# Kernel tuning notes

Measured on AMD Instinct MI355X. Metric: run time of the kernel, lower is better.

Reference implementation:

```python
import jax, jax.numpy as jnp
import numpy as np

B, C, H, W = 8, 128, 64, 64


def setup_inputs() -> dict:
    key = jax.random.key(0)
    ks = jax.random.split(key, 7)
    query_img = jax.random.normal(ks[0], (B, C, H, W), dtype=jnp.float32)
    key_img = jax.random.normal(ks[1], (B, C, H, W), dtype=jnp.float32)
    value_img = jax.random.normal(ks[2], (B, C, H, W), dtype=jnp.float32)
    # 1x1 conv weights == dense [out, in] matrices (kaiming-ish scale)
    scale = 1.0 / np.sqrt(C)
    Wq = jax.random.normal(ks[3], (C, C), dtype=jnp.float32) * scale
    bq = jax.random.normal(ks[4], (C,), dtype=jnp.float32) * scale
    Wk = jax.random.normal(ks[5], (C, C), dtype=jnp.float32) * scale
    bk = jax.random.normal(ks[6], (C,), dtype=jnp.float32) * scale
    return {"query_img": query_img, "key_img": key_img, "value_img": value_img,
            "Wq": Wq, "bq": bq, "Wk": Wk, "bk": bk}


def reference(query_img, key_img, value_img, Wq, bq, Wk, bk):
    b, c, h, w = query_img.shape
    hw = h * w
    # 1x1 convs as GEMMs -> token-major layout (b, hw, c_out)
    q = jnp.einsum('bchw,oc->bhwo', query_img, Wq).reshape(b, hw, -1) + bq
    k = jnp.einsum('bchw,oc->bohw', key_img, Wk).reshape(b, -1, hw) + bk[None, :, None]
    # scores scaled by sqrt(HW) (faithful: key.size(-1) == h*w in source)
    scores = jnp.einsum('bqc,bck->bqk', q, k) / jnp.sqrt(jnp.float32(hw))
    attn = jax.nn.softmax(scores, axis=-1)  # (b, hw, hw)
    v = value_img.reshape(b, c, hw).transpose(0, 2, 1)  # (b, hw, c)
    out = jnp.einsum('bqk,bkc->bqc', attn, v)  # (b, hw, c)
    out = out.transpose(0, 2, 1).reshape(b, -1, h, w)
    out = out + q.transpose(0, 2, 1).reshape(b, -1, h, w)  # residual from query proj
    return out
```

## Files before the change

kernel.cpp:

```cpp
#include <hip/hip_runtime.h>

#define BB 8
#define CC 128
#define SS 4096
#define KT 64
#define SCALE 0.015625f

typedef __attribute__((ext_vector_type(8))) short sh8;
typedef __attribute__((ext_vector_type(4))) float f32x4;

__device__ __forceinline__ float b2f(unsigned short u) {
    union { unsigned int i; float f; } x; x.i = ((unsigned int)u) << 16; return x.f;
}
__device__ __forceinline__ unsigned short f2b(float f) {
    union { float f; unsigned int i; } x; x.f = f;
    unsigned int r = x.i + 0x7fff + ((x.i >> 16) & 1);
    return (unsigned short)(r >> 16);
}
__device__ __forceinline__ unsigned short rhu(float f) {
    union { float f; unsigned int i; } x; x.f = f;
    return (unsigned short)((x.i + 0x8000) >> 16);
}

__device__ __forceinline__ void dma16(const void* g, void* l) {
    __builtin_amdgcn_global_load_lds((const __attribute__((address_space(1))) void*)g,
                                     (__attribute__((address_space(3))) void*)l,
                                     16, 0, 0);
}

__global__ __launch_bounds__(256) void cvt_kernel(
    const float* __restrict__ vimg,
    const float* __restrict__ Wq, const float* __restrict__ Wk,
    const float* __restrict__ bq, const float* __restrict__ bk,
    unsigned short* __restrict__ Vbuf,
    unsigned short* __restrict__ Wqb, unsigned short* __restrict__ Wkb,
    unsigned short* __restrict__ bqb, unsigned short* __restrict__ bkb)
{
    const int bx = blockIdx.x, tid = threadIdx.x;
    if (bx < 512) {
        const size_t base = (size_t)bx * 8192 + tid * 4;
        #pragma unroll
        for (int it = 0; it < 8; ++it) {
            const size_t i = base + (size_t)it * 1024;
            float4 v = *(const float4*)(vimg + i);
            ushort4 o;
            o.x = f2b(v.x); o.y = f2b(v.y); o.z = f2b(v.z); o.w = f2b(v.w);
            *(ushort4*)(Vbuf + i) = o;
        }
    } else {
        const int w = bx - 512;
        for (int e = w * 256 + tid; e < 33024; e += 2048) {
            float v; unsigned short* dst;
            if (e < 16384)      { v = Wq[e];         dst = Wqb + e; }
            else if (e < 32768) { v = Wk[e - 16384]; dst = Wkb + (e - 16384); }
            else if (e < 32896) { v = bq[e - 32768]; dst = bqb + (e - 32768); }
            else                { v = bk[e - 32896]; dst = bkb + (e - 32896); }
            *dst = f2b(v);
        }
    }
}

__global__ __launch_bounds__(256) void proj_kernel(
    const float* __restrict__ qimg, const float* __restrict__ kimg,
    const unsigned short* __restrict__ Wqb, const unsigned short* __restrict__ Wkb,
    const unsigned short* __restrict__ bqb, const unsigned short* __restrict__ bkb,
    unsigned short* __restrict__ Qbuf, unsigned short* __restrict__ Kbuf)
{
    __shared__ float ilds[128 * 69];

    const int z = blockIdx.z;
    const float* img = (z == 0) ? qimg : kimg;
    const unsigned short* Wb = (z == 0) ? Wqb : Wkb;
    const unsigned short* bias = (z == 0) ? bqb : bkb;
    unsigned short* outTok = (z == 0) ? Qbuf : Kbuf;

    const int tid  = threadIdx.x;
    const int wave = tid >> 6;
    const int lane = tid & 63;
    const int l15  = lane & 15;
    const int quad = lane >> 4;
    const int b     = blockIdx.y;
    const int stile = blockIdx.x;

    const float* gbase = img + (size_t)b * CC * SS + stile * 64;
    #pragma unroll
    for (int i = 0; i < 8; ++i) {
        const int l = tid + 256 * i;
        const int row = l >> 4, col = (l & 15) * 4;
        float4 v = *(const float4*)(gbase + (size_t)row * SS + col);
        float* d = ilds + row * 69 + col;
        d[0] = v.x; d[1] = v.y; d[2] = v.z; d[3] = v.w;
    }
    __syncthreads();

    const int tcol = wave * 16 + l15;
    sh8 a[4];
    #pragma unroll
    for (int kk = 0; kk < 4; ++kk)
        #pragma unroll
        for (int j = 0; j < 8; ++j)
            a[kk][j] = (short)rhu(ilds[(32 * kk + quad * 8 + j) * 69 + tcol]);

    f32x4 acc[8];
    #pragma unroll
    for (int nt = 0; nt < 8; ++nt) acc[nt] = (f32x4){0.f, 0.f, 0.f, 0.f};

    #pragma unroll
    for (int nt = 0; nt < 8; ++nt) {
        const unsigned short* wp = Wb + (size_t)(16 * nt + l15) * CC + quad * 8;
        #pragma unroll
        for (int kk = 0; kk < 4; ++kk) {
            sh8 bf = *(const sh8*)(wp + 32 * kk);
            acc[nt] = __builtin_amdgcn_mfma_f32_16x16x32_bf16(a[kk], bf, acc[nt], 0, 0, 0);
        }
    }

    #pragma unroll
    for (int nt = 0; nt < 8; ++nt) {
        const int o = 16 * nt + l15;
        const float bv = b2f(bias[o]);
        #pragma unroll
        for (int r = 0; r < 4; ++r) {
            const int s = stile * 64 + wave * 16 + quad * 4 + r;
            outTok[((size_t)b * SS + s) * CC + o] = f2b(acc[nt][r] + bv);
        }
    }
}

__global__ __launch_bounds__(256, 4) void attn_kernel(
    const unsigned short* __restrict__ Qbuf,
    const unsigned short* __restrict__ Kbuf,
    const unsigned short* __restrict__ Vbuf,
    float* __restrict__ out)
{
    __shared__ __align__(16) unsigned char smem[40960];
    unsigned char* kb = smem;
    unsigned char* vb = smem + 16384;

    const int tid  = threadIdx.x;
    const int wave = tid >> 6;
    const int lane = tid & 63;
    const int l15  = lane & 15;
    const int quad = lane >> 4;
    const int b     = blockIdx.y;
    const int qtile = blockIdx.x;
    const int qbase = qtile * 64 + wave * 16;

    unsigned char* pw = smem + 32768 + wave * 2048;

    const unsigned short* kbp = Kbuf + (size_t)b * SS * CC;
    const unsigned short* vbp = Vbuf + (size_t)b * CC * SS;

    sh8 aq[4];
    {
        const unsigned short* qp = Qbuf + ((size_t)b * SS + qbase + l15) * CC + quad * 8;
        #pragma unroll
        for (int kk = 0; kk < 4; ++kk) aq[kk] = *(const sh8*)(qp + 32 * kk);
    }

    int kGO[4], vGO[4];
    #pragma unroll
    for (int j = 0; j < 4; ++j) {
        const int krow = wave * 16 + j * 4 + (lane >> 4);
        kGO[j] = krow * 256 + (((lane & 15) ^ (krow & 7)) << 4);
        const int vrow = (wave * 4 + j) * 8 + (lane >> 3);
        vGO[j] = vrow * 8192 + (((lane & 7) ^ ((lane >> 3) & 7)) << 4);
    }

    f32x4 oacc[8];
    #pragma unroll
    for (int ct = 0; ct < 8; ++ct) oacc[ct] = (f32x4){0.f, 0.f, 0.f, 0.f};
    float lsum[4] = {0.f, 0.f, 0.f, 0.f};

    #pragma unroll
    for (int j = 0; j < 4; ++j) {
        dma16((const char*)kbp + kGO[j], kb + (wave * 4 + j) * 1024);
        dma16((const char*)vbp + vGO[j], vb + (wave * 4 + j) * 1024);
    }

    for (int it = 0; it < SS / KT; ++it) {
        __syncthreads();

        f32x4 sacc[4];
        #pragma unroll
        for (int n = 0; n < 4; ++n) {
            sacc[n] = (f32x4){0.f, 0.f, 0.f, 0.f};
            #pragma unroll
            for (int kk = 0; kk < 4; ++kk) {
                sh8 kf = *(const sh8*)(kb + (16 * n + l15) * 256
                                          + (((4 * kk + quad) ^ (l15 & 7)) << 4));
                sacc[n] = __builtin_amdgcn_mfma_f32_16x16x32_bf16(aq[kk], kf, sacc[n], 0, 0, 0);
            }
        }

        #pragma unroll
        for (int n = 0; n < 4; ++n)
            #pragma unroll
            for (int r = 0; r < 4; ++r) {
                float p = __expf(sacc[n][r] * SCALE);
                lsum[r] += p;
                const int row = quad * 4 + r, col = 16 * n + l15;
                *(unsigned short*)(pw + row * 128
                                   + (((col >> 3) ^ (row & 7)) << 4)
                                   + (col & 7) * 2) = rhu(p);
            }

        sh8 ap0 = *(const sh8*)(pw + l15 * 128 + ((quad ^ (l15 & 7)) << 4));
        #pragma unroll
        for (int ct = 0; ct < 8; ++ct) {
            sh8 bv = *(const sh8*)(vb + (16 * ct + l15) * 128
                                      + ((quad ^ (l15 & 7)) << 4));
            oacc[ct] = __builtin_amdgcn_mfma_f32_16x16x32_bf16(ap0, bv, oacc[ct], 0, 0, 0);
        }

        sh8 ap1 = *(const sh8*)(pw + l15 * 128 + (((4 + quad) ^ (l15 & 7)) << 4));
        sh8 vv[8];
        #pragma unroll
        for (int ct = 0; ct < 8; ++ct)
            vv[ct] = *(const sh8*)(vb + (16 * ct + l15) * 128
                                      + (((4 + quad) ^ (l15 & 7)) << 4));

        __syncthreads();

        if (it + 1 < SS / KT) {
            const char* gk = (const char*)kbp + (size_t)(it + 1) * KT * 256;
            const char* gv = (const char*)vbp + (size_t)(it + 1) * KT * 2;
            #pragma unroll
            for (int j = 0; j < 4; ++j) {
                dma16(gk + kGO[j], kb + (wave * 4 + j) * 1024);
                dma16(gv + vGO[j], vb + (wave * 4 + j) * 1024);
            }
        }

        #pragma unroll
        for (int ct = 0; ct < 8; ++ct)
            oacc[ct] = __builtin_amdgcn_mfma_f32_16x16x32_bf16(ap1, vv[ct], oacc[ct], 0, 0, 0);
    }

    #pragma unroll
    for (int r = 0; r < 4; ++r) {
        float v = lsum[r];
        #pragma unroll
        for (int m = 8; m >= 1; m >>= 1) v += __shfl_xor(v, m, 64);
        lsum[r] = v;
    }

    float (*oLds)[129] = (float(*)[129])smem;
    #pragma unroll
    for (int ct = 0; ct < 8; ++ct) {
        const int c = 16 * ct + l15;
        #pragma unroll
        for (int r = 0; r < 4; ++r) {
            const int qloc  = wave * 16 + quad * 4 + r;
            const int qglob = qtile * 64 + qloc;
            const float resid = b2f(Qbuf[((size_t)b * SS + qglob) * CC + c]);
            oLds[qloc][c] = oacc[ct][r] / lsum[r] + resid;
        }
    }
    __syncthreads();
    for (int idx = tid; idx < 64 * 128; idx += 256) {
        const int c = idx >> 6, q = idx & 63;
        out[((size_t)b * CC + c) * SS + qtile * 64 + q] = oLds[q][c];
    }
}

extern "C" void kernel_launch(void* const* d_in, const int* in_sizes, int n_in,
                              void* d_out, int out_size, void* d_ws, size_t ws_size,
                              hipStream_t stream) {
    const float* qimg = (const float*)d_in[0];
    const float* kimg = (const float*)d_in[1];
    const float* vimg = (const float*)d_in[2];
    const float* Wq   = (const float*)d_in[3];
    const float* bq   = (const float*)d_in[4];
    const float* Wk   = (const float*)d_in[5];
    const float* bk   = (const float*)d_in[6];
    float* out = (float*)d_out;

    unsigned short* Qbuf = (unsigned short*)d_ws;
    unsigned short* Kbuf = Qbuf + (size_t)BB * SS * CC;
    unsigned short* Vbuf = Kbuf + (size_t)BB * SS * CC;
    unsigned short* Wqb  = Vbuf + (size_t)BB * SS * CC;
    unsigned short* Wkb  = Wqb + CC * CC;
    unsigned short* bqb  = Wkb + CC * CC;
    unsigned short* bkb  = bqb + CC;

    cvt_kernel<<<dim3(520), 256, 0, stream>>>(vimg, Wq, Wk, bq, bk,
                                              Vbuf, Wqb, Wkb, bqb, bkb);
    proj_kernel<<<dim3(SS / 64, BB, 2), 256, 0, stream>>>(
        qimg, kimg, Wqb, Wkb, bqb, bkb, Qbuf, Kbuf);
    attn_kernel<<<dim3(SS / 64, BB), 256, 0, stream>>>(Qbuf, Kbuf, Vbuf, out);
}
```

Measured before the change: 224.8 us.

## Split attention key range across two blocks and merge with ticket-based reduction

Attention now splits the key/value sequence into two halves, one per block along grid z, which doubles the grid from 512 to 1024 blocks for better occupancy. Each block writes its partial bf16 output and row sums to workspace. A per-tile atomic ticket lets the second finisher combine both partials, normalise, add the residual and write the output. The weight/bias conversion kernel is folded into the projection kernel, which reads fp32 weights directly, and V conversion becomes a third z-slice of the same launch. This removes one launch but adds a memset, extra partial-output traffic and a bf16 rounding of the partial accumulators.

New measurement: 404.6 us. 80.0% more time.

```diff
diff --git a/kernel.cpp b/kernel.cpp
--- a/kernel.cpp
+++ b/kernel.cpp
@@ -4,6 +4,9 @@
 #define CC 128
 #define SS 4096
 #define KT 64
+#define NSPLIT 2
+#define HALF (SS / NSPLIT)
+#define ITERS (HALF / KT)
 #define SCALE 0.015625f
 
 typedef __attribute__((ext_vector_type(8))) short sh8;
@@ -28,17 +31,19 @@
                                      16, 0, 0);
 }
 
-__global__ __launch_bounds__(256) void cvt_kernel(
+__global__ __launch_bounds__(256) void aux_kernel(
+    const float* __restrict__ qimg, const float* __restrict__ kimg,
     const float* __restrict__ vimg,
-    const float* __restrict__ Wq, const float* __restrict__ Wk,
-    const float* __restrict__ bq, const float* __restrict__ bk,
-    unsigned short* __restrict__ Vbuf,
-    unsigned short* __restrict__ Wqb, unsigned short* __restrict__ Wkb,
-    unsigned short* __restrict__ bqb, unsigned short* __restrict__ bkb)
+    const float* __restrict__ Wq, const float* __restrict__ bq,
+    const float* __restrict__ Wk, const float* __restrict__ bk,
+    unsigned short* __restrict__ Qbuf, unsigned short* __restrict__ Kbuf,
+    unsigned short* __restrict__ Vbuf)
 {
-    const int bx = blockIdx.x, tid = threadIdx.x;
-    if (bx < 512) {
-        const size_t base = (size_t)bx * 8192 + tid * 4;
+    const int tid = threadIdx.x;
+    const int z   = blockIdx.z;
+
+    if (z == 2) {
+        const size_t base = ((size_t)blockIdx.y * 64 + blockIdx.x) * 8192 + tid * 4;
         #pragma unroll
         for (int it = 0; it < 8; ++it) {
             const size_t i = base + (size_t)it * 1024;
@@ -47,34 +52,16 @@
             o.x = f2b(v.x); o.y = f2b(v.y); o.z = f2b(v.z); o.w = f2b(v.w);
             *(ushort4*)(Vbuf + i) = o;
         }
-    } else {
-        const int w = bx - 512;
-        for (int e = w * 256 + tid; e < 33024; e += 2048) {
-            float v; unsigned short* dst;
-            if (e < 16384)      { v = Wq[e];         dst = Wqb + e; }
-            else if (e < 32768) { v = Wk[e - 16384]; dst = Wkb + (e - 16384); }
-            else if (e < 32896) { v = bq[e - 32768]; dst = bqb + (e - 32768); }
-            else                { v = bk[e - 32896]; dst = bkb + (e - 32896); }
-            *dst = f2b(v);
-        }
-    }
-}
-
-__global__ __launch_bounds__(256) void proj_kernel(
-    const float* __restrict__ qimg, const float* __restrict__ kimg,
-    const unsigned short* __restrict__ Wqb, const unsigned short* __restrict__ Wkb,
-    const unsigned short* __restrict__ bqb, const unsigned short* __restrict__ bkb,
-    unsigned short* __restrict__ Qbuf, unsigned short* __restrict__ Kbuf)
-{
+        return;
+    }
+
     __shared__ float ilds[128 * 69];
 
-    const int z = blockIdx.z;
-    const float* img = (z == 0) ? qimg : kimg;
-    const unsigned short* Wb = (z == 0) ? Wqb : Wkb;
-    const unsigned short* bias = (z == 0) ? bqb : bkb;
+    const float* img  = (z == 0) ? qimg : kimg;
+    const float* Wf   = (z == 0) ? Wq : Wk;
+    const float* bias = (z == 0) ? bq : bk;
     unsigned short* outTok = (z == 0) ? Qbuf : Kbuf;
 
-    const int tid  = threadIdx.x;
     const int wave = tid >> 6;
     const int lane = tid & 63;
     const int l15  = lane & 15;
@@ -107,18 +94,24 @@
 
     #pragma unroll
     for (int nt = 0; nt < 8; ++nt) {
-        const unsigned short* wp = Wb + (size_t)(16 * nt + l15) * CC + quad * 8;
+        const float* wp = Wf + (size_t)(16 * nt + l15) * CC + quad * 8;
         #pragma unroll
         for (int kk = 0; kk < 4; ++kk) {
-            sh8 bf = *(const sh8*)(wp + 32 * kk);
-            acc[nt] = __builtin_amdgcn_mfma_f32_16x16x32_bf16(a[kk], bf, acc[nt], 0, 0, 0);
+            float4 w0 = *(const float4*)(wp + 32 * kk);
+            float4 w1 = *(const float4*)(wp + 32 * kk + 4);
+            sh8 bfr;
+            bfr[0] = (short)rhu(w0.x); bfr[1] = (short)rhu(w0.y);
+            bfr[2] = (short)rhu(w0.z); bfr[3] = (short)rhu(w0.w);
+            bfr[4] = (short)rhu(w1.x); bfr[5] = (short)rhu(w1.y);
+            bfr[6] = (short)rhu(w1.z); bfr[7] = (short)rhu(w1.w);
+            acc[nt] = __builtin_amdgcn_mfma_f32_16x16x32_bf16(a[kk], bfr, acc[nt], 0, 0, 0);
         }
     }
 
     #pragma unroll
     for (int nt = 0; nt < 8; ++nt) {
         const int o = 16 * nt + l15;
-        const float bv = b2f(bias[o]);
+        const float bv = bias[o];
         #pragma unroll
         for (int r = 0; r < 4; ++r) {
             const int s = stile * 64 + wave * 16 + quad * 4 + r;
@@ -131,6 +124,9 @@
     const unsigned short* __restrict__ Qbuf,
     const unsigned short* __restrict__ Kbuf,
     const unsigned short* __restrict__ Vbuf,
+    unsigned short* __restrict__ pO,
+    float* __restrict__ pl,
+    int* __restrict__ tickets,
     float* __restrict__ out)
 {
     __shared__ __align__(16) unsigned char smem[40960];
@@ -144,12 +140,13 @@
     const int quad = lane >> 4;
     const int b     = blockIdx.y;
     const int qtile = blockIdx.x;
+    const int split = blockIdx.z;
     const int qbase = qtile * 64 + wave * 16;
 
     unsigned char* pw = smem + 32768 + wave * 2048;
 
-    const unsigned short* kbp = Kbuf + (size_t)b * SS * CC;
-    const unsigned short* vbp = Vbuf + (size_t)b * CC * SS;
+    const unsigned short* kbp = Kbuf + (size_t)b * SS * CC + (size_t)split * HALF * CC;
+    const unsigned short* vbp = Vbuf + (size_t)b * CC * SS + split * HALF;
 
     sh8 aq[4];
     {
@@ -178,7 +175,7 @@
         dma16((const char*)vbp + vGO[j], vb + (wave * 4 + j) * 1024);
     }
 
-    for (int it = 0; it < SS / KT; ++it) {
+    for (int it = 0; it < ITERS; ++it) {
         __syncthreads();
 
         f32x4 sacc[4];
@@ -222,7 +219,7 @@
 
         __syncthreads();
 
-        if (it + 1 < SS / KT) {
+        if (it + 1 < ITERS) {
             const char* gk = (const char*)kbp + (size_t)(it + 1) * KT * 256;
             const char* gv = (const char*)vbp + (size_t)(it + 1) * KT * 2;
             #pragma unroll
@@ -245,6 +242,35 @@
         lsum[r] = v;
     }
 
+    const int id = b * 64 + qtile;
+    unsigned short* myO = pO + ((size_t)(split * 512 + id)) * 8192;
+    #pragma unroll
+    for (int ct = 0; ct < 8; ++ct)
+        #pragma unroll
+        for (int r = 0; r < 4; ++r)
+            myO[(wave * 16 + quad * 4 + r) * 128 + 16 * ct + l15] = rhu(oacc[ct][r]);
+    if (l15 == 0)
+        #pragma unroll
+        for (int r = 0; r < 4; ++r)
+            pl[(split * 512 + id) * 64 + wave * 16 + quad * 4 + r] = lsum[r];
+
+    __threadfence();
+    __syncthreads();
+    int* flg = (int*)smem;
+    if (tid == 0) *flg = atomicAdd(&tickets[id], 1);
+    __syncthreads();
+    if (*flg == 0) return;
+
+    __threadfence();
+    __syncthreads();
+
+    const unsigned short* oO = pO + ((size_t)((1 - split) * 512 + id)) * 8192;
+    const float* opl = pl + ((1 - split) * 512 + id) * 64;
+    float ltot[4];
+    #pragma unroll
+    for (int r = 0; r < 4; ++r)
+        ltot[r] = lsum[r] + opl[wave * 16 + quad * 4 + r];
+
     float (*oLds)[129] = (float(*)[129])smem;
     #pragma unroll
     for (int ct = 0; ct < 8; ++ct) {
@@ -253,8 +279,9 @@
         for (int r = 0; r < 4; ++r) {
             const int qloc  = wave * 16 + quad * 4 + r;
             const int qglob = qtile * 64 + qloc;
+            const float o2 = b2f(oO[qloc * 128 + c]);
             const float resid = b2f(Qbuf[((size_t)b * SS + qglob) * CC + c]);
-            oLds[qloc][c] = oacc[ct][r] / lsum[r] + resid;
+            oLds[qloc][c] = (oacc[ct][r] + o2) / ltot[r] + resid;
         }
     }
     __syncthreads();
@@ -279,14 +306,13 @@
     unsigned short* Qbuf = (unsigned short*)d_ws;
     unsigned short* Kbuf = Qbuf + (size_t)BB * SS * CC;
     unsigned short* Vbuf = Kbuf + (size_t)BB * SS * CC;
-    unsigned short* Wqb  = Vbuf + (size_t)BB * SS * CC;
-    unsigned short* Wkb  = Wqb + CC * CC;
-    unsigned short* bqb  = Wkb + CC * CC;
-    unsigned short* bkb  = bqb + CC;
-
-    cvt_kernel<<<dim3(520), 256, 0, stream>>>(vimg, Wq, Wk, bq, bk,
-                                              Vbuf, Wqb, Wkb, bqb, bkb);
-    proj_kernel<<<dim3(SS / 64, BB, 2), 256, 0, stream>>>(
-        qimg, kimg, Wqb, Wkb, bqb, bkb, Qbuf, Kbuf);
-    attn_kernel<<<dim3(SS / 64, BB), 256, 0, stream>>>(Qbuf, Kbuf, Vbuf, out);
-}
+    unsigned short* pO   = Vbuf + (size_t)BB * SS * CC;
+    float* pl            = (float*)(pO + (size_t)2 * 512 * 8192);
+    int* tickets         = (int*)(pl + 2 * 512 * 64);
+
+    hipMemsetAsync(tickets, 0, 512 * sizeof(int), stream);
+    aux_kernel<<<dim3(SS / 64, BB, 3), 256, 0, stream>>>(
+        qimg, kimg, vimg, Wq, bq, Wk, bk, Qbuf, Kbuf, Vbuf);
+    attn_kernel<<<dim3(SS / 64, BB, NSPLIT), 256, 0, stream>>>(
+        Qbuf, Kbuf, Vbuf, pO, pl, tickets, out);
+}
```
